# Kernel optimization log

Hardware: AMD Instinct MI355X
Metric: run time of the kernel (lower is better)

The kernel has to match this reference:

```python
import jax, jax.numpy as jnp
import numpy as np


def _gather_nbrs(feats, idx):
    # feats: [C, N], idx: [N, k] -> [C, N, k]
    return feats[:, idx]


def pointconv_dw(xyz, feats, idx, w_pos, b_pos, w_out, b_out):
    """Depthwise point conv: per-channel weights from relative neighbor coords.
    xyz: [B,3,N], feats: [B,C,N], idx: [B,N,k] -> [B,C_out,N]
    """
    nbr_xyz = jax.vmap(_gather_nbrs)(xyz, idx)            # [B,3,N,k]
    rel = nbr_xyz - xyz[:, :, :, None]                    # relative positions
    w = jnp.einsum('cd,bdnk->bcnk', w_pos, rel) + b_pos[None, :, None, None]
    g = jax.vmap(_gather_nbrs)(feats, idx)                # [B,C,N,k]
    agg = jnp.sum(w * g, axis=-1)                         # [B,C,N] depthwise reduce over k
    return jnp.einsum('oc,bcn->bon', w_out, agg) + b_out[None, :, None]


def setup_inputs() -> dict:
    key = jax.random.key(0)
    ks = jax.random.split(key, 16)
    B, N, K = 2, 65536, 4
    IN, HID = 64, 64
    C = HID + IN
    s = 0.02
    inp = {
        'xyz': jax.random.normal(ks[0], (B, 3, N), jnp.float32),
        'h': jax.random.normal(ks[1], (B, HID, N), jnp.float32),
        'x': jax.random.normal(ks[2], (B, IN, N), jnp.float32),
        'knn_indices': jax.random.randint(ks[3], (B, N, K), 0, N, jnp.int32),
    }
    names = ['z', 'r', 'q']
    for i, nm in enumerate(names):
        inp[f'w{nm}_pos'] = s * jax.random.normal(ks[4 + 4 * i], (C, 3), jnp.float32)
        inp[f'b{nm}_pos'] = jnp.zeros((C,), jnp.float32)
        inp[f'w{nm}_out'] = s * jax.random.normal(ks[5 + 4 * i], (HID, C), jnp.float32)
        inp[f'b{nm}_out'] = jnp.zeros((HID,), jnp.float32)
    return inp


def reference(xyz, h, x, knn_indices,
              wz_pos, bz_pos, wz_out, bz_out,
              wr_pos, br_pos, wr_out, br_out,
              wq_pos, bq_pos, wq_out, bq_out):
    hx = jnp.concatenate([h, x], axis=1)                  # [B, HID+IN, N]
    z = jax.nn.sigmoid(pointconv_dw(xyz, hx, knn_indices, wz_pos, bz_pos, wz_out, bz_out))
    r = jax.nn.sigmoid(pointconv_dw(xyz, hx, knn_indices, wr_pos, br_pos, wr_out, br_out))
    rhx = jnp.concatenate([r * h, x], axis=1)
    q = jnp.tanh(pointconv_dw(xyz, rhx, knn_indices, wq_pos, bq_pos, wq_out, bq_out))
    return (1.0 - z) * h + z * q
```

## Files before the change

kernel.cpp:

```cpp
#include <hip/hip_runtime.h>

#define NPTS 65536
#define BATCH 2
#define CCH 128
#define HIDC 64
#define LDB 520
#define LDB2 264
#define PLD 130

typedef unsigned short u16;
typedef unsigned int u32;
typedef __bf16 bf16_t;
typedef bf16_t bf16x8 __attribute__((ext_vector_type(8)));
typedef float f32x4 __attribute__((ext_vector_type(4)));

__device__ __forceinline__ u16 f2bf(float f){
  union { float f; unsigned u; } v; v.f = f;
  unsigned r = v.u + 0x7FFFu + ((v.u >> 16) & 1u);
  return (u16)(r >> 16);
}
__device__ __forceinline__ float bf2f(u16 u){
  union { unsigned u; float f; } v; v.u = ((unsigned)u) << 16; return v.f;
}
__device__ __forceinline__ u32 pkrn(float a, float b){
  union { float f; u32 u; } ua, ub; ua.f = a; ub.f = b;
  return ((ua.u + 0x8000u) >> 16) | ((ub.u + 0x8000u) & 0xffff0000u);
}
__device__ __forceinline__ float sigmoidf_(float v){ return 1.f/(1.f+__expf(-v)); }
__device__ __forceinline__ float tanhf_(float v){
  v = fminf(10.f, fmaxf(-10.f, v));
  float e = __expf(2.f*v);
  return (e-1.f)/(e+1.f);
}

__global__ __launch_bounds__(256) void kprep(
    const float* __restrict__ wz, const float* __restrict__ wzp, const float* __restrict__ bzp,
    const float* __restrict__ wr, const float* __restrict__ wrp, const float* __restrict__ brp,
    const float* __restrict__ wq, const float* __restrict__ wqp, const float* __restrict__ bqp,
    u16* __restrict__ A){
  int idx = blockIdx.x*256 + threadIdx.x;
  if (idx < 98304){
    int t = idx & 7, o = (idx>>3)&63, quad = (idx>>9)&3, s = (idx>>11)&15, g = idx>>15;
    int pk = s*32 + quad*8 + t;
    int j = pk>>7, chunk = (pk>>3)&15, tt = pk&7;
    int orig = chunk*32 + j*8 + tt;
    int c = orig>>2, m = orig&3;
    const float* W  = (g==0)? wz  : (g==1)? wr  : wq;
    const float* wp = (g==0)? wzp : (g==1)? wrp : wqp;
    const float* bp = (g==0)? bzp : (g==1)? brp : bqp;
    float coef = m ? wp[c*3 + m - 1] : bp[c];
    A[idx] = f2bf(W[o*CCH + c] * coef);
  } else {
    int i2 = idx - 98304;
    int t = i2 & 7, o = (i2>>3)&63, quad = (i2>>9)&3, s = (i2>>11)&7;
    int k2 = s*32 + quad*8 + t;
    int j = k2>>6, chunk = (k2>>3)&7, tt = k2&7;
    int orig = chunk*32 + j*8 + tt;
    int c = orig>>2, m = orig&3;
    float coef = m ? wqp[c*3 + m - 1] : bqp[c];
    A[idx] = f2bf(wq[o*CCH + c] * coef);
  }
}

__global__ __launch_bounds__(256) void k_pack(const float* __restrict__ h,
    const float* __restrict__ x, u16* __restrict__ hxT){
  __shared__ __align__(16) u16 tile[64*PLD];
  int tid = threadIdx.x;
  int b = blockIdx.x >> 10, n0 = (blockIdx.x & 1023) << 6;
  #pragma unroll
  for (int i = 0; i < 8; ++i){
    int cc = (tid>>4) + i*16;
    int nn = (tid & 15)*4;
    const float* src = (cc < HIDC)
        ? (h + (((size_t)(b*HIDC + cc))<<16) + n0 + nn)
        : (x + (((size_t)(b*HIDC + cc - HIDC))<<16) + n0 + nn);
    float4 v = *(const float4*)src;
    tile[(nn+0)*PLD + cc] = f2bf(v.x);
    tile[(nn+1)*PLD + cc] = f2bf(v.y);
    tile[(nn+2)*PLD + cc] = f2bf(v.z);
    tile[(nn+3)*PLD + cc] = f2bf(v.w);
  }
  __syncthreads();
  #pragma unroll
  for (int i = 0; i < 4; ++i){
    int tsk = tid + (i<<8);
    int n = tsk>>4, ch = (tsk&15)*8;
    uint4 v = *(const uint4*)(tile + n*PLD + ch);
    *(uint4*)(hxT + (((size_t)(b<<16) + n0 + n)<<7) + ch) = v;
  }
}

#define ACCUM(gv, rv) { \
  u32 dw_[4] = {gv.x, gv.y, gv.z, gv.w}; \
  _Pragma("unroll") \
  for (int q_ = 0; q_ < 4; ++q_){ \
    union { u32 u; float f; } lo_, hi_; \
    lo_.u = dw_[q_] << 16; hi_.u = dw_[q_] & 0xffff0000u; \
    m0[2*q_]   += lo_.f; mx[2*q_]   += rv.x*lo_.f; my[2*q_]   += rv.y*lo_.f; mz[2*q_]   += rv.z*lo_.f; \
    m0[2*q_+1] += hi_.f; mx[2*q_+1] += rv.x*hi_.f; my[2*q_+1] += rv.y*hi_.f; mz[2*q_+1] += rv.z*hi_.f; \
  } }

#define PACKROW(row, CHOFF, STRIDE) { \
  _Pragma("unroll") \
  for (int j_ = 0; j_ < 4; ++j_){ \
    int ca_ = 2*j_, cb_ = 2*j_+1; \
    uint4 v_; \
    v_.x = pkrn(m0[ca_], mx[ca_]); v_.y = pkrn(my[ca_], mz[ca_]); \
    v_.z = pkrn(m0[cb_], mx[cb_]); v_.w = pkrn(my[cb_], mz[cb_]); \
    *(uint4*)((row) + j_*(STRIDE) + (CHOFF)) = v_; \
  } }

__global__ __launch_bounds__(256, 4) void k_zr(
    const float* __restrict__ xyz, const float* __restrict__ h,
    const int* __restrict__ knn,
    const float* __restrict__ bz_out, const float* __restrict__ br_out,
    const u16* __restrict__ Azr,
    const u16* __restrict__ hxT, u16* __restrict__ rhT,
    u16* __restrict__ z_ws, u16* __restrict__ qx_ws)
{
  __shared__ __align__(16) u16 bext[32*LDB];
  __shared__ __align__(16) float4 relk[128];
  __shared__ __align__(16) int4 jlds[32];

  int tid = threadIdx.x; int lane = tid & 63; int wv = tid >> 6;
  int b = blockIdx.x >> 11, n0 = (blockIdx.x & 2047) << 5;
  size_t bN = (size_t)b * NPTS;

  if (tid < 128){
    int p = tid >> 2, k = tid & 3;
    int j = knn[((bN + n0 + p) << 2) + k];
    ((int*)jlds)[tid] = j;
    const float* xb = xyz + (size_t)b*3*NPTS;
    float cx = xb[n0+p], cy = xb[NPTS + n0+p], cz = xb[2*NPTS + n0+p];
    relk[tid] = make_float4(xb[j]-cx, xb[NPTS+j]-cy, xb[2*NPTS+j]-cz, 0.f);
  }
  __syncthreads();

  const u16* hxTb = hxT + (bN << 7);
  int pA = tid >> 4, chk = tid & 15;
  int pB = pA + 16;
  int4 jA = jlds[pA], jB = jlds[pB];
  const u16* cb = hxTb + chk*8;
  uint4 ga0 = *(const uint4*)(cb + (((size_t)jA.x)<<7));
  uint4 ga1 = *(const uint4*)(cb + (((size_t)jA.y)<<7));
  uint4 ga2 = *(const uint4*)(cb + (((size_t)jA.z)<<7));
  uint4 ga3 = *(const uint4*)(cb + (((size_t)jA.w)<<7));
  uint4 gb0 = *(const uint4*)(cb + (((size_t)jB.x)<<7));
  uint4 gb1 = *(const uint4*)(cb + (((size_t)jB.y)<<7));
  uint4 gb2 = *(const uint4*)(cb + (((size_t)jB.z)<<7));
  uint4 gb3 = *(const uint4*)(cb + (((size_t)jB.w)<<7));
  {
    float4 r0 = relk[pA*4+0], r1 = relk[pA*4+1], r2 = relk[pA*4+2], r3 = relk[pA*4+3];
    float m0[8] = {0,0,0,0,0,0,0,0}, mx[8] = {0,0,0,0,0,0,0,0};
    float my[8] = {0,0,0,0,0,0,0,0}, mz[8] = {0,0,0,0,0,0,0,0};
    ACCUM(ga0, r0); ACCUM(ga1, r1); ACCUM(ga2, r2); ACCUM(ga3, r3);
    PACKROW(bext + pA*LDB, chk*8, 128);
  }
  {
    float4 r0 = relk[pB*4+0], r1 = relk[pB*4+1], r2 = relk[pB*4+2], r3 = relk[pB*4+3];
    float m0[8] = {0,0,0,0,0,0,0,0}, mx[8] = {0,0,0,0,0,0,0,0};
    float my[8] = {0,0,0,0,0,0,0,0}, mz[8] = {0,0,0,0,0,0,0,0};
    ACCUM(gb0, r0); ACCUM(gb1, r1); ACCUM(gb2, r2); ACCUM(gb3, r3);
    PACKROW(bext + pB*LDB, chk*8, 128);
  }
  __syncthreads();

  int l15 = lane & 15, quad = lane >> 4;
  int orow = wv*16 + l15;
  f32x4 accz[2], accr[2], accq[2];
  #pragma unroll
  for (int nt = 0; nt < 2; ++nt){
    accz[nt] = (f32x4){0,0,0,0}; accr[nt] = (f32x4){0,0,0,0}; accq[nt] = (f32x4){0,0,0,0};
  }
  #pragma unroll
  for (int s = 0; s < 16; ++s){
    bf16x8 az = *(const bf16x8*)(Azr + ((s*4 + quad)*64 + orow)*8);
    bf16x8 ar = *(const bf16x8*)(Azr + 32768 + ((s*4 + quad)*64 + orow)*8);
    if (s & 2){
      bf16x8 aq = *(const bf16x8*)(Azr + 65536 + ((s*4 + quad)*64 + orow)*8);
      #pragma unroll
      for (int nt = 0; nt < 2; ++nt){
        bf16x8 bb = *(const bf16x8*)(bext + (nt*16 + l15)*LDB + s*32 + quad*8);
        accz[nt] = __builtin_amdgcn_mfma_f32_16x16x32_bf16(az, bb, accz[nt], 0, 0, 0);
        accr[nt] = __builtin_amdgcn_mfma_f32_16x16x32_bf16(ar, bb, accr[nt], 0, 0, 0);
        accq[nt] = __builtin_amdgcn_mfma_f32_16x16x32_bf16(aq, bb, accq[nt], 0, 0, 0);
      }
    } else {
      #pragma unroll
      for (int nt = 0; nt < 2; ++nt){
        bf16x8 bb = *(const bf16x8*)(bext + (nt*16 + l15)*LDB + s*32 + quad*8);
        accz[nt] = __builtin_amdgcn_mfma_f32_16x16x32_bf16(az, bb, accz[nt], 0, 0, 0);
        accr[nt] = __builtin_amdgcn_mfma_f32_16x16x32_bf16(ar, bb, accr[nt], 0, 0, 0);
      }
    }
  }
  __syncthreads();

  u16* zst  = bext;
  u16* rhst = bext + 2560;
  u16* qxst = bext + 2560 + 2304;
  #pragma unroll
  for (int nt = 0; nt < 2; ++nt){
    #pragma unroll
    for (int reg = 0; reg < 4; ++reg){
      int o = wv*16 + quad*4 + reg;
      int p = nt*16 + l15;
      float zf = sigmoidf_(accz[nt][reg] + bz_out[o]);
      float rf = sigmoidf_(accr[nt][reg] + br_out[o]);
      float hv = h[(((size_t)(b*HIDC + o))<<16) + n0 + p];
      zst[o*40 + p] = f2bf(zf);
      rhst[p*72 + o] = f2bf(rf * hv);
      qxst[o*40 + p] = f2bf(accq[nt][reg]);
    }
  }
  __syncthreads();

  {
    int p = tid >> 3, ch = (tid & 7)*8;
    uint4 v = *(const uint4*)(rhst + p*72 + ch);
    *(uint4*)(rhT + ((bN + n0 + p)<<6) + ch) = v;
  }
  {
    int o = tid >> 2, pc = (tid & 3)*8;
    uint4 v = *(const uint4*)(zst + o*40 + pc);
    *(uint4*)(z_ws + (((size_t)(b*HIDC + o))<<16) + n0 + pc) = v;
  }
  {
    int o = tid >> 2, pc = (tid & 3)*8;
    uint4 v = *(const uint4*)(qxst + o*40 + pc);
    *(uint4*)(qx_ws + (((size_t)(b*HIDC + o))<<16) + n0 + pc) = v;
  }
}

__global__ __launch_bounds__(256, 4) void k_q(
    const float* __restrict__ xyz, const float* __restrict__ h,
    const int* __restrict__ knn,
    const float* __restrict__ bq_out,
    const u16* __restrict__ Aqrh,
    const u16* __restrict__ rhT, const u16* __restrict__ z_ws,
    const u16* __restrict__ qx_ws, float* __restrict__ out)
{
  __shared__ __align__(16) u16 bext[64*LDB2];
  __shared__ __align__(16) float4 relk[256];
  __shared__ __align__(16) int4 jlds[64];

  int tid = threadIdx.x; int lane = tid & 63; int wv = tid >> 6;
  int b = blockIdx.x >> 10, n0 = (blockIdx.x & 1023) << 6;
  size_t bN = (size_t)b * NPTS;

  {
    int p = tid >> 2, k = tid & 3;
    int j = knn[((bN + n0 + p) << 2) + k];
    ((int*)jlds)[tid] = j;
    const float* xb = xyz + (size_t)b*3*NPTS;
    float cx = xb[n0+p], cy = xb[NPTS + n0+p], cz = xb[2*NPTS + n0+p];
    relk[tid] = make_float4(xb[j]-cx, xb[NPTS+j]-cy, xb[2*NPTS+j]-cz, 0.f);
  }
  __syncthreads();

  const u16* rhTb = rhT + (bN << 6);
  int pA = tid >> 3, chk = tid & 7;
  int pB = pA + 32;
  int4 jA = jlds[pA], jB = jlds[pB];
  const u16* cb = rhTb + chk*8;
  uint4 ga0 = *(const uint4*)(cb + (((size_t)jA.x)<<6));
  uint4 ga1 = *(const uint4*)(cb + (((size_t)jA.y)<<6));
  uint4 ga2 = *(const uint4*)(cb + (((size_t)jA.z)<<6));
  uint4 ga3 = *(const uint4*)(cb + (((size_t)jA.w)<<6));
  uint4 gb0 = *(const uint4*)(cb + (((size_t)jB.x)<<6));
  uint4 gb1 = *(const uint4*)(cb + (((size_t)jB.y)<<6));
  uint4 gb2 = *(const uint4*)(cb + (((size_t)jB.z)<<6));
  uint4 gb3 = *(const uint4*)(cb + (((size_t)jB.w)<<6));
  {
    float4 r0 = relk[pA*4+0], r1 = relk[pA*4+1], r2 = relk[pA*4+2], r3 = relk[pA*4+3];
    float m0[8] = {0,0,0,0,0,0,0,0}, mx[8] = {0,0,0,0,0,0,0,0};
    float my[8] = {0,0,0,0,0,0,0,0}, mz[8] = {0,0,0,0,0,0,0,0};
    ACCUM(ga0, r0); ACCUM(ga1, r1); ACCUM(ga2, r2); ACCUM(ga3, r3);
    PACKROW(bext + pA*LDB2, chk*8, 64);
  }
  {
    float4 r0 = relk[pB*4+0], r1 = relk[pB*4+1], r2 = relk[pB*4+2], r3 = relk[pB*4+3];
    float m0[8] = {0,0,0,0,0,0,0,0}, mx[8] = {0,0,0,0,0,0,0,0};
    float my[8] = {0,0,0,0,0,0,0,0}, mz[8] = {0,0,0,0,0,0,0,0};
    ACCUM(gb0, r0); ACCUM(gb1, r1); ACCUM(gb2, r2); ACCUM(gb3, r3);
    PACKROW(bext + pB*LDB2, chk*8, 64);
  }
  __syncthreads();

  int l15 = lane & 15, quad = lane >> 4;
  int orow = wv*16 + l15;
  f32x4 acc[4];
  #pragma unroll
  for (int nt = 0; nt < 4; ++nt) acc[nt] = (f32x4){0,0,0,0};
  #pragma unroll
  for (int s = 0; s < 8; ++s){
    bf16x8 aq = *(const bf16x8*)(Aqrh + ((s*4 + quad)*64 + orow)*8);
    #pragma unroll
    for (int nt = 0; nt < 4; ++nt){
      bf16x8 bb = *(const bf16x8*)(bext + (nt*16 + l15)*LDB2 + s*32 + quad*8);
      acc[nt] = __builtin_amdgcn_mfma_f32_16x16x32_bf16(aq, bb, acc[nt], 0, 0, 0);
    }
  }

  #pragma unroll
  for (int nt = 0; nt < 4; ++nt){
    #pragma unroll
    for (int reg = 0; reg < 4; ++reg){
      int o = wv*16 + quad*4 + reg;
      int p = nt*16 + l15;
      size_t idx = (((size_t)(b*HIDC + o))<<16) + n0 + p;
      float qpre = acc[nt][reg] + bq_out[o] + bf2f(qx_ws[idx]);
      float qf = tanhf_(qpre);
      float zf = bf2f(z_ws[idx]);
      float hv = h[idx];
      out[idx] = (1.f - zf)*hv + zf*qf;
    }
  }
}

extern "C" void kernel_launch(void* const* d_in, const int* in_sizes, int n_in,
                              void* d_out, int out_size, void* d_ws, size_t ws_size,
                              hipStream_t stream){
  const float* xyz    = (const float*)d_in[0];
  const float* h      = (const float*)d_in[1];
  const float* x      = (const float*)d_in[2];
  const int*   knn    = (const int*)d_in[3];
  const float* wz_pos = (const float*)d_in[4];
  const float* bz_pos = (const float*)d_in[5];
  const float* wz_out = (const float*)d_in[6];
  const float* bz_out = (const float*)d_in[7];
  const float* wr_pos = (const float*)d_in[8];
  const float* br_pos = (const float*)d_in[9];
  const float* wr_out = (const float*)d_in[10];
  const float* br_out = (const float*)d_in[11];
  const float* wq_pos = (const float*)d_in[12];
  const float* bq_pos = (const float*)d_in[13];
  const float* wq_out = (const float*)d_in[14];
  const float* bq_out = (const float*)d_in[15];
  float* out = (float*)d_out;

  u16* ws    = (u16*)d_ws;
  u16* hxT   = ws;
  u16* rhT   = ws + 16777216;
  u16* z_ws  = ws + 25165824;
  u16* qx_ws = ws + 33554432;
  u16* A     = ws + 41943040;

  kprep<<<448, 256, 0, stream>>>(wz_out, wz_pos, bz_pos, wr_out, wr_pos, br_pos,
                                 wq_out, wq_pos, bq_pos, A);
  k_pack<<<2048, 256, 0, stream>>>(h, x, hxT);
  k_zr<<<4096, 256, 0, stream>>>(xyz, h, knn, bz_out, br_out, A, hxT, rhT, z_ws, qx_ws);
  k_q<<<2048, 256, 0, stream>>>(xyz, h, knn, bq_out, A + 98304, rhT, z_ws, qx_ws, out);
}
```

Before: 224.2 us.

## Halve points per block in both conv kernels and use packed float2 accumulation

Both k_zr and k_q now process half as many points per block (16 and 32), with grids doubled and launch bounds raised to 8 blocks per SIMD-level occupancy hint. The gather/accumulate step uses two-wide float vectors so the compiler can emit packed FMA instructions. The goal is more waves in flight to hide the latency of the random neighbor gathers, and less register and LDS use per block. In exchange, the MFMA A-fragment weight loads are amortized over fewer point tiles, so more weight traffic per point, and the tighter register cap may cause spills.

```diff
diff --git a/kernel.cpp b/kernel.cpp
--- a/kernel.cpp
+++ b/kernel.cpp
@@ -13,6 +13,7 @@
 typedef __bf16 bf16_t;
 typedef bf16_t bf16x8 __attribute__((ext_vector_type(8)));
 typedef float f32x4 __attribute__((ext_vector_type(4)));
+typedef float f32x2 __attribute__((ext_vector_type(2)));
 
 __device__ __forceinline__ u16 f2bf(float f){
   union { float f; unsigned u; } v; v.f = f;
@@ -96,21 +97,20 @@
   for (int q_ = 0; q_ < 4; ++q_){ \
     union { u32 u; float f; } lo_, hi_; \
     lo_.u = dw_[q_] << 16; hi_.u = dw_[q_] & 0xffff0000u; \
-    m0[2*q_]   += lo_.f; mx[2*q_]   += rv.x*lo_.f; my[2*q_]   += rv.y*lo_.f; mz[2*q_]   += rv.z*lo_.f; \
-    m0[2*q_+1] += hi_.f; mx[2*q_+1] += rv.x*hi_.f; my[2*q_+1] += rv.y*hi_.f; mz[2*q_+1] += rv.z*hi_.f; \
+    f32x2 v_ = {lo_.f, hi_.f}; \
+    m0[q_] += v_; mx[q_] += rv.x * v_; my[q_] += rv.y * v_; mz[q_] += rv.z * v_; \
   } }
 
 #define PACKROW(row, CHOFF, STRIDE) { \
   _Pragma("unroll") \
   for (int j_ = 0; j_ < 4; ++j_){ \
-    int ca_ = 2*j_, cb_ = 2*j_+1; \
     uint4 v_; \
-    v_.x = pkrn(m0[ca_], mx[ca_]); v_.y = pkrn(my[ca_], mz[ca_]); \
-    v_.z = pkrn(m0[cb_], mx[cb_]); v_.w = pkrn(my[cb_], mz[cb_]); \
+    v_.x = pkrn(m0[j_].x, mx[j_].x); v_.y = pkrn(my[j_].x, mz[j_].x); \
+    v_.z = pkrn(m0[j_].y, mx[j_].y); v_.w = pkrn(my[j_].y, mz[j_].y); \
     *(uint4*)((row) + j_*(STRIDE) + (CHOFF)) = v_; \
   } }
 
-__global__ __launch_bounds__(256, 4) void k_zr(
+__global__ __launch_bounds__(256, 8) void k_zr(
     const float* __restrict__ xyz, const float* __restrict__ h,
     const int* __restrict__ knn,
     const float* __restrict__ bz_out, const float* __restrict__ br_out,
@@ -118,7 +118,97 @@
     const u16* __restrict__ hxT, u16* __restrict__ rhT,
     u16* __restrict__ z_ws, u16* __restrict__ qx_ws)
 {
-  __shared__ __align__(16) u16 bext[32*LDB];
+  __shared__ __align__(16) u16 bext[16*LDB];
+  __shared__ __align__(16) float4 relk[64];
+  __shared__ __align__(16) int4 jlds[16];
+
+  int tid = threadIdx.x; int lane = tid & 63; int wv = tid >> 6;
+  int b = blockIdx.x >> 12, n0 = (blockIdx.x & 4095) << 4;
+  size_t bN = (size_t)b * NPTS;
+
+  if (tid < 64){
+    int p = tid >> 2, k = tid & 3;
+    int j = knn[((bN + n0 + p) << 2) + k];
+    ((int*)jlds)[tid] = j;
+    const float* xb = xyz + (size_t)b*3*NPTS;
+    float cx = xb[n0+p], cy = xb[NPTS + n0+p], cz = xb[2*NPTS + n0+p];
+    relk[tid] = make_float4(xb[j]-cx, xb[NPTS+j]-cy, xb[2*NPTS+j]-cz, 0.f);
+  }
+  __syncthreads();
+
+  const u16* hxTb = hxT + (bN << 7);
+  int pA = tid >> 4, chk = tid & 15;
+  int4 jA = jlds[pA];
+  const u16* cb = hxTb + chk*8;
+  uint4 ga0 = *(const uint4*)(cb + (((size_t)jA.x)<<7));
+  uint4 ga1 = *(const uint4*)(cb + (((size_t)jA.y)<<7));
+  uint4 ga2 = *(const uint4*)(cb + (((size_t)jA.z)<<7));
+  uint4 ga3 = *(const uint4*)(cb + (((size_t)jA.w)<<7));
+  {
+    float4 r0 = relk[pA*4+0], r1 = relk[pA*4+1], r2 = relk[pA*4+2], r3 = relk[pA*4+3];
+    f32x2 m0[4] = {{0,0},{0,0},{0,0},{0,0}}, mx[4] = {{0,0},{0,0},{0,0},{0,0}};
+    f32x2 my[4] = {{0,0},{0,0},{0,0},{0,0}}, mz[4] = {{0,0},{0,0},{0,0},{0,0}};
+    ACCUM(ga0, r0); ACCUM(ga1, r1); ACCUM(ga2, r2); ACCUM(ga3, r3);
+    PACKROW(bext + pA*LDB, chk*8, 128);
+  }
+  __syncthreads();
+
+  int l15 = lane & 15, quad = lane >> 4;
+  int orow = wv*16 + l15;
+  f32x4 accz = (f32x4){0,0,0,0}, accr = (f32x4){0,0,0,0}, accq = (f32x4){0,0,0,0};
+  #pragma unroll
+  for (int s = 0; s < 16; ++s){
+    bf16x8 az = *(const bf16x8*)(Azr + ((s*4 + quad)*64 + orow)*8);
+    bf16x8 ar = *(const bf16x8*)(Azr + 32768 + ((s*4 + quad)*64 + orow)*8);
+    bf16x8 bb = *(const bf16x8*)(bext + l15*LDB + s*32 + quad*8);
+    accz = __builtin_amdgcn_mfma_f32_16x16x32_bf16(az, bb, accz, 0, 0, 0);
+    accr = __builtin_amdgcn_mfma_f32_16x16x32_bf16(ar, bb, accr, 0, 0, 0);
+    if (s & 2){
+      bf16x8 aq = *(const bf16x8*)(Azr + 65536 + ((s*4 + quad)*64 + orow)*8);
+      accq = __builtin_amdgcn_mfma_f32_16x16x32_bf16(aq, bb, accq, 0, 0, 0);
+    }
+  }
+  __syncthreads();
+
+  u16* zst  = bext;
+  u16* rhst = bext + 1536;
+  u16* qxst = bext + 2688;
+  #pragma unroll
+  for (int reg = 0; reg < 4; ++reg){
+    int o = wv*16 + quad*4 + reg;
+    int p = l15;
+    float zf = sigmoidf_(accz[reg] + bz_out[o]);
+    float rf = sigmoidf_(accr[reg] + br_out[o]);
+    float hv = h[(((size_t)(b*HIDC + o))<<16) + n0 + p];
+    zst[o*24 + p] = f2bf(zf);
+    rhst[p*72 + o] = f2bf(rf * hv);
+    qxst[o*24 + p] = f2bf(accq[reg]);
+  }
+  __syncthreads();
+
+  if (tid < 128){
+    int p = tid >> 3, ch = (tid & 7)*8;
+    uint4 v = *(const uint4*)(rhst + p*72 + ch);
+    *(uint4*)(rhT + ((bN + n0 + p)<<6) + ch) = v;
+  }
+  {
+    int o = tid >> 2, hl = (tid >> 1) & 1, pc = (tid & 1)*8;
+    const u16* src = hl ? qxst : zst;
+    u16* dst = hl ? qx_ws : z_ws;
+    uint4 v = *(const uint4*)(src + o*24 + pc);
+    *(uint4*)(dst + (((size_t)(b*HIDC + o))<<16) + n0 + pc) = v;
+  }
+}
+
+__global__ __launch_bounds__(256, 8) void k_q(
+    const float* __restrict__ xyz, const float* __restrict__ h,
+    const int* __restrict__ knn,
+    const float* __restrict__ bq_out,
+    const u16* __restrict__ Aqrh,
+    const u16* __restrict__ rhT, const u16* __restrict__ z_ws,
+    const u16* __restrict__ qx_ws, float* __restrict__ out)
+{
+  __shared__ __align__(16) u16 bext[32*LDB2];
   __shared__ __align__(16) float4 relk[128];
   __shared__ __align__(16) int4 jlds[32];
 
@@ -136,174 +226,40 @@
   }
   __syncthreads();
 
-  const u16* hxTb = hxT + (bN << 7);
-  int pA = tid >> 4, chk = tid & 15;
-  int pB = pA + 16;
-  int4 jA = jlds[pA], jB = jlds[pB];
-  const u16* cb = hxTb + chk*8;
-  uint4 ga0 = *(const uint4*)(cb + (((size_t)jA.x)<<7));
-  uint4 ga1 = *(const uint4*)(cb + (((size_t)jA.y)<<7));
-  uint4 ga2 = *(const uint4*)(cb + (((size_t)jA.z)<<7));
-  uint4 ga3 = *(const uint4*)(cb + (((size_t)jA.w)<<7));
-  uint4 gb0 = *(const uint4*)(cb + (((size_t)jB.x)<<7));
-  uint4 gb1 = *(const uint4*)(cb + (((size_t)jB.y)<<7));
-  uint4 gb2 = *(const uint4*)(cb + (((size_t)jB.z)<<7));
-  uint4 gb3 = *(const uint4*)(cb + (((size_t)jB.w)<<7));
-  {
-    float4 r0 = relk[pA*4+0], r1 = relk[pA*4+1], r2 = relk[pA*4+2], r3 = relk[pA*4+3];
-    float m0[8] = {0,0,0,0,0,0,0,0}, mx[8] = {0,0,0,0,0,0,0,0};
-    float my[8] = {0,0,0,0,0,0,0,0}, mz[8] = {0,0,0,0,0,0,0,0};
-    ACCUM(ga0, r0); ACCUM(ga1, r1); ACCUM(ga2, r2); ACCUM(ga3, r3);
-    PACKROW(bext + pA*LDB, chk*8, 128);
-  }
-  {
-    float4 r0 = relk[pB*4+0], r1 = relk[pB*4+1], r2 = relk[pB*4+2], r3 = relk[pB*4+3];
-    float m0[8] = {0,0,0,0,0,0,0,0}, mx[8] = {0,0,0,0,0,0,0,0};
-    float my[8] = {0,0,0,0,0,0,0,0}, mz[8] = {0,0,0,0,0,0,0,0};
-    ACCUM(gb0, r0); ACCUM(gb1, r1); ACCUM(gb2, r2); ACCUM(gb3, r3);
-    PACKROW(bext + pB*LDB, chk*8, 128);
-  }
-  __syncthreads();
-
-  int l15 = lane & 15, quad = lane >> 4;
-  int orow = wv*16 + l15;
-  f32x4 accz[2], accr[2], accq[2];
-  #pragma unroll
-  for (int nt = 0; nt < 2; ++nt){
-    accz[nt] = (f32x4){0,0,0,0}; accr[nt] = (f32x4){0,0,0,0}; accq[nt] = (f32x4){0,0,0,0};
-  }
-  #pragma unroll
-  for (int s = 0; s < 16; ++s){
-    bf16x8 az = *(const bf16x8*)(Azr + ((s*4 + quad)*64 + orow)*8);
-    bf16x8 ar = *(const bf16x8*)(Azr + 32768 + ((s*4 + quad)*64 + orow)*8);
-    if (s & 2){
-      bf16x8 aq = *(const bf16x8*)(Azr + 65536 + ((s*4 + quad)*64 + orow)*8);
-      #pragma unroll
-      for (int nt = 0; nt < 2; ++nt){
-        bf16x8 bb = *(const bf16x8*)(bext + (nt*16 + l15)*LDB + s*32 + quad*8);
-        accz[nt] = __builtin_amdgcn_mfma_f32_16x16x32_bf16(az, bb, accz[nt], 0, 0, 0);
-        accr[nt] = __builtin_amdgcn_mfma_f32_16x16x32_bf16(ar, bb, accr[nt], 0, 0, 0);
-        accq[nt] = __builtin_amdgcn_mfma_f32_16x16x32_bf16(aq, bb, accq[nt], 0, 0, 0);
-      }
-    } else {
-      #pragma unroll
-      for (int nt = 0; nt < 2; ++nt){
-        bf16x8 bb = *(const bf16x8*)(bext + (nt*16 + l15)*LDB + s*32 + quad*8);
-        accz[nt] = __builtin_amdgcn_mfma_f32_16x16x32_bf16(az, bb, accz[nt], 0, 0, 0);
-        accr[nt] = __builtin_amdgcn_mfma_f32_16x16x32_bf16(ar, bb, accr[nt], 0, 0, 0);
-      }
-    }
-  }
-  __syncthreads();
-
-  u16* zst  = bext;
-  u16* rhst = bext + 2560;
-  u16* qxst = bext + 2560 + 2304;
-  #pragma unroll
-  for (int nt = 0; nt < 2; ++nt){
-    #pragma unroll
-    for (int reg = 0; reg < 4; ++reg){
-      int o = wv*16 + quad*4 + reg;
-      int p = nt*16 + l15;
-      float zf = sigmoidf_(accz[nt][reg] + bz_out[o]);
-      float rf = sigmoidf_(accr[nt][reg] + br_out[o]);
-      float hv = h[(((size_t)(b*HIDC + o))<<16) + n0 + p];
-      zst[o*40 + p] = f2bf(zf);
-      rhst[p*72 + o] = f2bf(rf * hv);
-      qxst[o*40 + p] = f2bf(accq[nt][reg]);
-    }
-  }
-  __syncthreads();
-
-  {
-    int p = tid >> 3, ch = (tid & 7)*8;
-    uint4 v = *(const uint4*)(rhst + p*72 + ch);
-    *(uint4*)(rhT + ((bN + n0 + p)<<6) + ch) = v;
-  }
-  {
-    int o = tid >> 2, pc = (tid & 3)*8;
-    uint4 v = *(const uint4*)(zst + o*40 + pc);
-    *(uint4*)(z_ws + (((size_t)(b*HIDC + o))<<16) + n0 + pc) = v;
-  }
-  {
-    int o = tid >> 2, pc = (tid & 3)*8;
-    uint4 v = *(const uint4*)(qxst + o*40 + pc);
-    *(uint4*)(qx_ws + (((size_t)(b*HIDC + o))<<16) + n0 + pc) = v;
-  }
-}
-
-__global__ __launch_bounds__(256, 4) void k_q(
-    const float* __restrict__ xyz, const float* __restrict__ h,
-    const int* __restrict__ knn,
-    const float* __restrict__ bq_out,
-    const u16* __restrict__ Aqrh,
-    const u16* __restrict__ rhT, const u16* __restrict__ z_ws,
-    const u16* __restrict__ qx_ws, float* __restrict__ out)
-{
-  __shared__ __align__(16) u16 bext[64*LDB2];
-  __shared__ __align__(16) float4 relk[256];
-  __shared__ __align__(16) int4 jlds[64];
-
-  int tid = threadIdx.x; int lane = tid & 63; int wv = tid >> 6;
-  int b = blockIdx.x >> 10, n0 = (blockIdx.x & 1023) << 6;
-  size_t bN = (size_t)b * NPTS;
-
-  {
-    int p = tid >> 2, k = tid & 3;
-    int j = knn[((bN + n0 + p) << 2) + k];
-    ((int*)jlds)[tid] = j;
-    const float* xb = xyz + (size_t)b*3*NPTS;
-    float cx = xb[n0+p], cy = xb[NPTS + n0+p], cz = xb[2*NPTS + n0+p];
-    relk[tid] = make_float4(xb[j]-cx, xb[NPTS+j]-cy, xb[2*NPTS+j]-cz, 0.f);
-  }
-  __syncthreads();
-
   const u16* rhTb = rhT + (bN << 6);
   int pA = tid >> 3, chk = tid & 7;
-  int pB = pA + 32;
-  int4 jA = jlds[pA], jB = jlds[pB];
+  int4 jA = jlds[pA];
   const u16* cb = rhTb + chk*8;
   uint4 ga0 = *(const uint4*)(cb + (((size_t)jA.x)<<6));
   uint4 ga1 = *(const uint4*)(cb + (((size_t)jA.y)<<6));
   uint4 ga2 = *(const uint4*)(cb + (((size_t)jA.z)<<6));
   uint4 ga3 = *(const uint4*)(cb + (((size_t)jA.w)<<6));
-  uint4 gb0 = *(const uint4*)(cb + (((size_t)jB.x)<<6));
-  uint4 gb1 = *(const uint4*)(cb + (((size_t)jB.y)<<6));
-  uint4 gb2 = *(const uint4*)(cb + (((size_t)jB.z)<<6));
-  uint4 gb3 = *(const uint4*)(cb + (((size_t)jB.w)<<6));
   {
     float4 r0 = relk[pA*4+0], r1 = relk[pA*4+1], r2 = relk[pA*4+2], r3 = relk[pA*4+3];
-    float m0[8] = {0,0,0,0,0,0,0,0}, mx[8] = {0,0,0,0,0,0,0,0};
-    float my[8] = {0,0,0,0,0,0,0,0}, mz[8] = {0,0,0,0,0,0,0,0};
+    f32x2 m0[4] = {{0,0},{0,0},{0,0},{0,0}}, mx[4] = {{0,0},{0,0},{0,0},{0,0}};
+    f32x2 my[4] = {{0,0},{0,0},{0,0},{0,0}}, mz[4] = {{0,0},{0,0},{0,0},{0,0}};
     ACCUM(ga0, r0); ACCUM(ga1, r1); ACCUM(ga2, r2); ACCUM(ga3, r3);
     PACKROW(bext + pA*LDB2, chk*8, 64);
   }
-  {
-    float4 r0 = relk[pB*4+0], r1 = relk[pB*4+1], r2 = relk[pB*4+2], r3 = relk[pB*4+3];
-    float m0[8] = {0,0,0,0,0,0,0,0}, mx[8] = {0,0,0,0,0,0,0,0};
-    float my[8] = {0,0,0,0,0,0,0,0}, mz[8] = {0,0,0,0,0,0,0,0};
-    ACCUM(gb0, r0); ACCUM(gb1, r1); ACCUM(gb2, r2); ACCUM(gb3, r3);
-    PACKROW(bext + pB*LDB2, chk*8, 64);
-  }
   __syncthreads();
 
   int l15 = lane & 15, quad = lane >> 4;
   int orow = wv*16 + l15;
-  f32x4 acc[4];
-  #pragma unroll
-  for (int nt = 0; nt < 4; ++nt) acc[nt] = (f32x4){0,0,0,0};
+  f32x4 acc[2];
+  #pragma unroll
+  for (int nt = 0; nt < 2; ++nt) acc[nt] = (f32x4){0,0,0,0};
   #pragma unroll
   for (int s = 0; s < 8; ++s){
     bf16x8 aq = *(const bf16x8*)(Aqrh + ((s*4 + quad)*64 + orow)*8);
     #pragma unroll
-    for (int nt = 0; nt < 4; ++nt){
+    for (int nt = 0; nt < 2; ++nt){
       bf16x8 bb = *(const bf16x8*)(bext + (nt*16 + l15)*LDB2 + s*32 + quad*8);
       acc[nt] = __builtin_amdgcn_mfma_f32_16x16x32_bf16(aq, bb, acc[nt], 0, 0, 0);
     }
   }
 
   #pragma unroll
-  for (int nt = 0; nt < 4; ++nt){
+  for (int nt = 0; nt < 2; ++nt){
     #pragma unroll
     for (int reg = 0; reg < 4; ++reg){
       int o = wv*16 + quad*4 + reg;
@@ -349,6 +305,6 @@
   kprep<<<448, 256, 0, stream>>>(wz_out, wz_pos, bz_pos, wr_out, wr_pos, br_pos,
                                  wq_out, wq_pos, bq_pos, A);
   k_pack<<<2048, 256, 0, stream>>>(h, x, hxT);
-  k_zr<<<4096, 256, 0, stream>>>(xyz, h, knn, bz_out, br_out, A, hxT, rhT, z_ws, qx_ws);
-  k_q<<<2048, 256, 0, stream>>>(xyz, h, knn, bq_out, A + 98304, rhT, z_ws, qx_ws, out);
-}
+  k_zr<<<8192, 256, 0, stream>>>(xyz, h, knn, bz_out, br_out, A, hxT, rhT, z_ws, qx_ws);
+  k_q<<<4096, 256, 0, stream>>>(xyz, h, knn, bq_out, A + 98304, rhT, z_ws, qx_ws, out);
+}
```

Measured after the change: 255.2 us. +13.9%, slower.

## Double k_zr point tile to 64 and vectorize moment accumulation as float2

Applied to the files above, without the earlier changes.

k_zr now processes 64 points per block instead of 32, halving the grid and letting each wave reuse the loaded A weight fragments across four MFMA column tiles instead of two. Each thread issues 16 neighbor gathers up front for more memory-level parallelism. The moment accumulation in both kernels switches to float2 vectors so the compiler can emit packed FP32 math. The trade-off is higher register and LDS use per block, and launch bounds are relaxed to 2 blocks per CU, which may reduce occupancy and latency hiding.

```diff
diff --git a/kernel.cpp b/kernel.cpp
--- a/kernel.cpp
+++ b/kernel.cpp
@@ -13,6 +13,7 @@
 typedef __bf16 bf16_t;
 typedef bf16_t bf16x8 __attribute__((ext_vector_type(8)));
 typedef float f32x4 __attribute__((ext_vector_type(4)));
+typedef float f32x2 __attribute__((ext_vector_type(2)));
 
 __device__ __forceinline__ u16 f2bf(float f){
   union { float f; unsigned u; } v; v.f = f;
@@ -96,21 +97,27 @@
   for (int q_ = 0; q_ < 4; ++q_){ \
     union { u32 u; float f; } lo_, hi_; \
     lo_.u = dw_[q_] << 16; hi_.u = dw_[q_] & 0xffff0000u; \
-    m0[2*q_]   += lo_.f; mx[2*q_]   += rv.x*lo_.f; my[2*q_]   += rv.y*lo_.f; mz[2*q_]   += rv.z*lo_.f; \
-    m0[2*q_+1] += hi_.f; mx[2*q_+1] += rv.x*hi_.f; my[2*q_+1] += rv.y*hi_.f; mz[2*q_+1] += rv.z*hi_.f; \
+    f32x2 v_ = {lo_.f, hi_.f}; \
+    m0[q_] += v_; mx[q_] += rv.x * v_; my[q_] += rv.y * v_; mz[q_] += rv.z * v_; \
   } }
 
 #define PACKROW(row, CHOFF, STRIDE) { \
   _Pragma("unroll") \
   for (int j_ = 0; j_ < 4; ++j_){ \
-    int ca_ = 2*j_, cb_ = 2*j_+1; \
     uint4 v_; \
-    v_.x = pkrn(m0[ca_], mx[ca_]); v_.y = pkrn(my[ca_], mz[ca_]); \
-    v_.z = pkrn(m0[cb_], mx[cb_]); v_.w = pkrn(my[cb_], mz[cb_]); \
+    v_.x = pkrn(m0[j_].x, mx[j_].x); v_.y = pkrn(my[j_].x, mz[j_].x); \
+    v_.z = pkrn(m0[j_].y, mx[j_].y); v_.w = pkrn(my[j_].y, mz[j_].y); \
     *(uint4*)((row) + j_*(STRIDE) + (CHOFF)) = v_; \
   } }
 
-__global__ __launch_bounds__(256, 4) void k_zr(
+#define MOMGRP(PP, GA, GB, GC, GD) { \
+  float4 r0 = relk[(PP)*4+0], r1 = relk[(PP)*4+1], r2 = relk[(PP)*4+2], r3 = relk[(PP)*4+3]; \
+  f32x2 m0[4] = {{0,0},{0,0},{0,0},{0,0}}, mx[4] = {{0,0},{0,0},{0,0},{0,0}}; \
+  f32x2 my[4] = {{0,0},{0,0},{0,0},{0,0}}, mz[4] = {{0,0},{0,0},{0,0},{0,0}}; \
+  ACCUM(GA, r0); ACCUM(GB, r1); ACCUM(GC, r2); ACCUM(GD, r3); \
+  PACKROW(bext + (PP)*LDB, chk*8, 128); }
+
+__global__ __launch_bounds__(256, 2) void k_zr(
     const float* __restrict__ xyz, const float* __restrict__ h,
     const int* __restrict__ knn,
     const float* __restrict__ bz_out, const float* __restrict__ br_out,
@@ -118,15 +125,15 @@
     const u16* __restrict__ hxT, u16* __restrict__ rhT,
     u16* __restrict__ z_ws, u16* __restrict__ qx_ws)
 {
-  __shared__ __align__(16) u16 bext[32*LDB];
-  __shared__ __align__(16) float4 relk[128];
-  __shared__ __align__(16) int4 jlds[32];
+  __shared__ __align__(16) u16 bext[64*LDB];
+  __shared__ __align__(16) float4 relk[256];
+  __shared__ __align__(16) int4 jlds[64];
 
   int tid = threadIdx.x; int lane = tid & 63; int wv = tid >> 6;
-  int b = blockIdx.x >> 11, n0 = (blockIdx.x & 2047) << 5;
+  int b = blockIdx.x >> 10, n0 = (blockIdx.x & 1023) << 6;
   size_t bN = (size_t)b * NPTS;
 
-  if (tid < 128){
+  {
     int p = tid >> 2, k = tid & 3;
     int j = knn[((bN + n0 + p) << 2) + k];
     ((int*)jlds)[tid] = j;
@@ -138,38 +145,35 @@
 
   const u16* hxTb = hxT + (bN << 7);
   int pA = tid >> 4, chk = tid & 15;
-  int pB = pA + 16;
-  int4 jA = jlds[pA], jB = jlds[pB];
   const u16* cb = hxTb + chk*8;
-  uint4 ga0 = *(const uint4*)(cb + (((size_t)jA.x)<<7));
-  uint4 ga1 = *(const uint4*)(cb + (((size_t)jA.y)<<7));
-  uint4 ga2 = *(const uint4*)(cb + (((size_t)jA.z)<<7));
-  uint4 ga3 = *(const uint4*)(cb + (((size_t)jA.w)<<7));
-  uint4 gb0 = *(const uint4*)(cb + (((size_t)jB.x)<<7));
-  uint4 gb1 = *(const uint4*)(cb + (((size_t)jB.y)<<7));
-  uint4 gb2 = *(const uint4*)(cb + (((size_t)jB.z)<<7));
-  uint4 gb3 = *(const uint4*)(cb + (((size_t)jB.w)<<7));
-  {
-    float4 r0 = relk[pA*4+0], r1 = relk[pA*4+1], r2 = relk[pA*4+2], r3 = relk[pA*4+3];
-    float m0[8] = {0,0,0,0,0,0,0,0}, mx[8] = {0,0,0,0,0,0,0,0};
-    float my[8] = {0,0,0,0,0,0,0,0}, mz[8] = {0,0,0,0,0,0,0,0};
-    ACCUM(ga0, r0); ACCUM(ga1, r1); ACCUM(ga2, r2); ACCUM(ga3, r3);
-    PACKROW(bext + pA*LDB, chk*8, 128);
-  }
-  {
-    float4 r0 = relk[pB*4+0], r1 = relk[pB*4+1], r2 = relk[pB*4+2], r3 = relk[pB*4+3];
-    float m0[8] = {0,0,0,0,0,0,0,0}, mx[8] = {0,0,0,0,0,0,0,0};
-    float my[8] = {0,0,0,0,0,0,0,0}, mz[8] = {0,0,0,0,0,0,0,0};
-    ACCUM(gb0, r0); ACCUM(gb1, r1); ACCUM(gb2, r2); ACCUM(gb3, r3);
-    PACKROW(bext + pB*LDB, chk*8, 128);
-  }
+  int4 j0 = jlds[pA], j1 = jlds[pA+16], j2 = jlds[pA+32], j3 = jlds[pA+48];
+  uint4 g00 = *(const uint4*)(cb + (((size_t)j0.x)<<7));
+  uint4 g01 = *(const uint4*)(cb + (((size_t)j0.y)<<7));
+  uint4 g02 = *(const uint4*)(cb + (((size_t)j0.z)<<7));
+  uint4 g03 = *(const uint4*)(cb + (((size_t)j0.w)<<7));
+  uint4 g10 = *(const uint4*)(cb + (((size_t)j1.x)<<7));
+  uint4 g11 = *(const uint4*)(cb + (((size_t)j1.y)<<7));
+  uint4 g12 = *(const uint4*)(cb + (((size_t)j1.z)<<7));
+  uint4 g13 = *(const uint4*)(cb + (((size_t)j1.w)<<7));
+  uint4 g20 = *(const uint4*)(cb + (((size_t)j2.x)<<7));
+  uint4 g21 = *(const uint4*)(cb + (((size_t)j2.y)<<7));
+  uint4 g22 = *(const uint4*)(cb + (((size_t)j2.z)<<7));
+  uint4 g23 = *(const uint4*)(cb + (((size_t)j2.w)<<7));
+  uint4 g30 = *(const uint4*)(cb + (((size_t)j3.x)<<7));
+  uint4 g31 = *(const uint4*)(cb + (((size_t)j3.y)<<7));
+  uint4 g32 = *(const uint4*)(cb + (((size_t)j3.z)<<7));
+  uint4 g33 = *(const uint4*)(cb + (((size_t)j3.w)<<7));
+  MOMGRP(pA,      g00, g01, g02, g03);
+  MOMGRP(pA + 16, g10, g11, g12, g13);
+  MOMGRP(pA + 32, g20, g21, g22, g23);
+  MOMGRP(pA + 48, g30, g31, g32, g33);
   __syncthreads();
 
   int l15 = lane & 15, quad = lane >> 4;
   int orow = wv*16 + l15;
-  f32x4 accz[2], accr[2], accq[2];
-  #pragma unroll
-  for (int nt = 0; nt < 2; ++nt){
+  f32x4 accz[4], accr[4], accq[4];
+  #pragma unroll
+  for (int nt = 0; nt < 4; ++nt){
     accz[nt] = (f32x4){0,0,0,0}; accr[nt] = (f32x4){0,0,0,0}; accq[nt] = (f32x4){0,0,0,0};
   }
   #pragma unroll
@@ -179,7 +183,7 @@
     if (s & 2){
       bf16x8 aq = *(const bf16x8*)(Azr + 65536 + ((s*4 + quad)*64 + orow)*8);
       #pragma unroll
-      for (int nt = 0; nt < 2; ++nt){
+      for (int nt = 0; nt < 4; ++nt){
         bf16x8 bb = *(const bf16x8*)(bext + (nt*16 + l15)*LDB + s*32 + quad*8);
         accz[nt] = __builtin_amdgcn_mfma_f32_16x16x32_bf16(az, bb, accz[nt], 0, 0, 0);
         accr[nt] = __builtin_amdgcn_mfma_f32_16x16x32_bf16(ar, bb, accr[nt], 0, 0, 0);
@@ -187,7 +191,7 @@
       }
     } else {
       #pragma unroll
-      for (int nt = 0; nt < 2; ++nt){
+      for (int nt = 0; nt < 4; ++nt){
         bf16x8 bb = *(const bf16x8*)(bext + (nt*16 + l15)*LDB + s*32 + quad*8);
         accz[nt] = __builtin_amdgcn_mfma_f32_16x16x32_bf16(az, bb, accz[nt], 0, 0, 0);
         accr[nt] = __builtin_amdgcn_mfma_f32_16x16x32_bf16(ar, bb, accr[nt], 0, 0, 0);
@@ -197,10 +201,10 @@
   __syncthreads();
 
   u16* zst  = bext;
-  u16* rhst = bext + 2560;
-  u16* qxst = bext + 2560 + 2304;
-  #pragma unroll
-  for (int nt = 0; nt < 2; ++nt){
+  u16* rhst = bext + 4608;
+  u16* qxst = bext + 9216;
+  #pragma unroll
+  for (int nt = 0; nt < 4; ++nt){
     #pragma unroll
     for (int reg = 0; reg < 4; ++reg){
       int o = wv*16 + quad*4 + reg;
@@ -208,27 +212,23 @@
       float zf = sigmoidf_(accz[nt][reg] + bz_out[o]);
       float rf = sigmoidf_(accr[nt][reg] + br_out[o]);
       float hv = h[(((size_t)(b*HIDC + o))<<16) + n0 + p];
-      zst[o*40 + p] = f2bf(zf);
+      zst[o*72 + p] = f2bf(zf);
       rhst[p*72 + o] = f2bf(rf * hv);
-      qxst[o*40 + p] = f2bf(accq[nt][reg]);
+      qxst[o*72 + p] = f2bf(accq[nt][reg]);
     }
   }
   __syncthreads();
 
-  {
-    int p = tid >> 3, ch = (tid & 7)*8;
-    uint4 v = *(const uint4*)(rhst + p*72 + ch);
-    *(uint4*)(rhT + ((bN + n0 + p)<<6) + ch) = v;
-  }
-  {
-    int o = tid >> 2, pc = (tid & 3)*8;
-    uint4 v = *(const uint4*)(zst + o*40 + pc);
-    *(uint4*)(z_ws + (((size_t)(b*HIDC + o))<<16) + n0 + pc) = v;
-  }
-  {
-    int o = tid >> 2, pc = (tid & 3)*8;
-    uint4 v = *(const uint4*)(qxst + o*40 + pc);
-    *(uint4*)(qx_ws + (((size_t)(b*HIDC + o))<<16) + n0 + pc) = v;
+  #pragma unroll
+  for (int i = 0; i < 2; ++i){
+    int t = tid + (i<<8);
+    int a = t >> 3, c8 = (t & 7)*8;
+    uint4 vr = *(const uint4*)(rhst + a*72 + c8);
+    *(uint4*)(rhT + ((bN + n0 + a)<<6) + c8) = vr;
+    uint4 vz = *(const uint4*)(zst + a*72 + c8);
+    *(uint4*)(z_ws + (((size_t)(b*HIDC + a))<<16) + n0 + c8) = vz;
+    uint4 vq = *(const uint4*)(qxst + a*72 + c8);
+    *(uint4*)(qx_ws + (((size_t)(b*HIDC + a))<<16) + n0 + c8) = vq;
   }
 }
 
@@ -273,15 +273,15 @@
   uint4 gb3 = *(const uint4*)(cb + (((size_t)jB.w)<<6));
   {
     float4 r0 = relk[pA*4+0], r1 = relk[pA*4+1], r2 = relk[pA*4+2], r3 = relk[pA*4+3];
-    float m0[8] = {0,0,0,0,0,0,0,0}, mx[8] = {0,0,0,0,0,0,0,0};
-    float my[8] = {0,0,0,0,0,0,0,0}, mz[8] = {0,0,0,0,0,0,0,0};
+    f32x2 m0[4] = {{0,0},{0,0},{0,0},{0,0}}, mx[4] = {{0,0},{0,0},{0,0},{0,0}};
+    f32x2 my[4] = {{0,0},{0,0},{0,0},{0,0}}, mz[4] = {{0,0},{0,0},{0,0},{0,0}};
     ACCUM(ga0, r0); ACCUM(ga1, r1); ACCUM(ga2, r2); ACCUM(ga3, r3);
     PACKROW(bext + pA*LDB2, chk*8, 64);
   }
   {
     float4 r0 = relk[pB*4+0], r1 = relk[pB*4+1], r2 = relk[pB*4+2], r3 = relk[pB*4+3];
-    float m0[8] = {0,0,0,0,0,0,0,0}, mx[8] = {0,0,0,0,0,0,0,0};
-    float my[8] = {0,0,0,0,0,0,0,0}, mz[8] = {0,0,0,0,0,0,0,0};
+    f32x2 m0[4] = {{0,0},{0,0},{0,0},{0,0}}, mx[4] = {{0,0},{0,0},{0,0},{0,0}};
+    f32x2 my[4] = {{0,0},{0,0},{0,0},{0,0}}, mz[4] = {{0,0},{0,0},{0,0},{0,0}};
     ACCUM(gb0, r0); ACCUM(gb1, r1); ACCUM(gb2, r2); ACCUM(gb3, r3);
     PACKROW(bext + pB*LDB2, chk*8, 64);
   }
@@ -349,6 +349,6 @@
   kprep<<<448, 256, 0, stream>>>(wz_out, wz_pos, bz_pos, wr_out, wr_pos, br_pos,
                                  wq_out, wq_pos, bq_pos, A);
   k_pack<<<2048, 256, 0, stream>>>(h, x, hxT);
-  k_zr<<<4096, 256, 0, stream>>>(xyz, h, knn, bz_out, br_out, A, hxT, rhT, z_ws, qx_ws);
+  k_zr<<<2048, 256, 0, stream>>>(xyz, h, knn, bz_out, br_out, A, hxT, rhT, z_ws, qx_ws);
   k_q<<<2048, 256, 0, stream>>>(xyz, h, knn, bq_out, A + 98304, rhT, z_ws, qx_ws, out);
 }
```

Result: slower. 232.2 us (+3.6%).
